# Performance work log

Measured on AMD Instinct MI355X. Metric: run time of the kernel, lower is better.

Reference implementation:

```python
import jax, jax.numpy as jnp
import numpy as np

N = 100_000        # nodes
E = 1_600_000      # edges (avg in-degree 16)
D_IN = 128
D_OUT = 128
K = 2              # hops


def setup_inputs() -> dict:
    key = jax.random.key(0)
    k1, k2, k3, k4 = jax.random.split(key, 4)
    feat = jax.random.normal(k1, (N, D_IN), dtype=jnp.float32)
    src = jax.random.randint(k2, (E,), 0, N, dtype=jnp.int64)
    # guarantee every node has in-degree >= 1 so deg**-0.5 is finite
    # (first N dst entries cover all nodes, rest random)
    dst_rand = jax.random.randint(k3, (E - N,), 0, N, dtype=jnp.int64)
    dst = jnp.concatenate([jnp.arange(N, dtype=jnp.int64), dst_rand])
    # xavier-normal-ish linear params: Linear(D_IN*(K+1) -> D_OUT)
    fan_in = D_IN * (K + 1)
    std = np.sqrt(2.0) * np.sqrt(2.0 / (fan_in + D_OUT))  # gain('relu') * xavier
    W = jax.random.normal(k4, (D_OUT, fan_in), dtype=jnp.float32) * std
    b = jnp.zeros((D_OUT,), dtype=jnp.float32)
    return {"feat": feat, "src": src, "dst": dst, "W": W, "b": b}


def reference(feat, src, dst, W, b):
    n = feat.shape[0]
    # in-degree based symmetric normalization: D^{-1/2} A D^{-1/2}
    deg = jax.ops.segment_sum(jnp.ones_like(dst, dtype=feat.dtype), dst,
                              num_segments=n)
    norm = (deg ** -0.5)[:, None]                 # [N, 1]
    fstack = [feat]
    h = feat
    for _ in range(K):
        h = h * norm                              # pre-scale by D^{-1/2}
        # SpMM: sum of source features into destination nodes
        h = jax.ops.segment_sum(h[src], dst, num_segments=n)
        h = h * norm                              # post-scale by D^{-1/2}
        fstack.append(h)
    x = jnp.concatenate(fstack, axis=-1)          # [N, D_IN*(K+1)]
    return x @ W.T + b
```

## Files before the change

kernel.cpp:

```cpp
#include <hip/hip_runtime.h>
#include <hip/hip_bf16.h>


#define D 128
#define TPB 256
#define GEMM_GRID 768

#define BSH 9
#define BSZ 512
#define NBMAX 256
#define EPT 16
#define CH (TPB * EPT)
#define LCAP 16384

typedef __attribute__((ext_vector_type(8))) short short8;
typedef __attribute__((ext_vector_type(4))) float f32x4;

__device__ __forceinline__ ushort f2bf(float f) {
    unsigned u = __float_as_uint(f);
    u += 0x7fff + ((u >> 16) & 1);
    return (ushort)(u >> 16);
}
__device__ __forceinline__ unsigned pack2bf(float x, float y) {
    return (unsigned)f2bf(x) | ((unsigned)f2bf(y) << 16);
}
__device__ __forceinline__ float bf_lo(unsigned v) { return __uint_as_float(v << 16); }
__device__ __forceinline__ float bf_hi(unsigned v) { return __uint_as_float(v & 0xffff0000u); }

__global__ __launch_bounds__(TPB) void mega_kernel(
    const int* __restrict__ src, const int* __restrict__ dst,
    int* __restrict__ gCursor, unsigned* __restrict__ tmp,
    const float* __restrict__ feat, unsigned* __restrict__ featb,
    const float* __restrict__ W, ushort* __restrict__ Wb,
    int e, int n, int nbin, int npre) {
    __shared__ int hist[NBMAX];
    __shared__ int cellBase[NBMAX];
    int t = threadIdx.x;
    int bid = blockIdx.x;

    if (bid < nbin) {
        hist[t] = 0;
        __syncthreads();
        int base = bid * CH;
        int b[EPT]; unsigned pk[EPT]; int r[EPT];
#pragma unroll
        for (int k = 0; k < EPT; ++k) {
            int i = base + k * TPB + t;
            b[k] = -1;
            if (i < e) {
                int d = dst[i];
                b[k] = d >> BSH;
                pk[k] = ((unsigned)src[i] << BSH) | (unsigned)(d & (BSZ - 1));
                r[k] = atomicAdd(&hist[b[k]], 1);
            }
        }
        __syncthreads();
        int h = hist[t];
        cellBase[t] = h ? t * LCAP + atomicAdd(&gCursor[t], h) : 0;
        __syncthreads();
#pragma unroll
        for (int k = 0; k < EPT; ++k)
            if (b[k] >= 0) tmp[cellBase[b[k]] + r[k]] = pk[k];
    } else if (bid < nbin + npre) {
        int gid = (bid - nbin) * TPB + t;
        int node = gid >> 6, c = gid & 63;
        if (node >= n) return;
        float2 f = ((const float2*)(feat + (size_t)node * D))[c];
        featb[(size_t)node * 64 + c] = pack2bf(f.x, f.y);
    } else {
        int i = ((bid - nbin - npre) * TPB + t) * 4;
        float4 w = *(const float4*)(W + i);
        ushort4 o;
        o.x = f2bf(w.x); o.y = f2bf(w.y); o.z = f2bf(w.z); o.w = f2bf(w.w);
        *(ushort4*)(Wb + i) = o;
    }
}

__global__ __launch_bounds__(TPB) void bucket_csr_kernel(
    const unsigned* __restrict__ tmp, const int* __restrict__ gCursor,
    int2* __restrict__ rsdeg, float* __restrict__ norm, int* __restrict__ csr,
    int n) {
    __shared__ int cnt[BSZ];
    __shared__ int off[BSZ];
    __shared__ int pr[TPB];
    __shared__ int lcsr[LCAP];
    int t = threadIdx.x;
    int bkt = blockIdx.x;
    int beg = bkt * LCAP;
    int m = gCursor[bkt];
    int end = beg + m;
    cnt[t] = 0; cnt[t + TPB] = 0;
    __syncthreads();
    for (int i = beg + t; i < end; i += TPB)
        atomicAdd(&cnt[tmp[i] & (BSZ - 1)], 1);
    __syncthreads();
    int c0 = cnt[2 * t], c1 = cnt[2 * t + 1];
    int own = c0 + c1;
    pr[t] = own;
    __syncthreads();
    for (int o = 1; o < TPB; o <<= 1) {
        int x = (t >= o) ? pr[t - o] : 0;
        __syncthreads();
        pr[t] += x;
        __syncthreads();
    }
    int ex = pr[t] - own;
    off[2 * t] = ex;
    off[2 * t + 1] = ex + c0;
    __syncthreads();
    cnt[t] = 0; cnt[t + TPB] = 0;
    __syncthreads();
    for (int i = beg + t; i < end; i += TPB) {
        unsigned v = tmp[i];
        int l = v & (BSZ - 1);
        int r = atomicAdd(&cnt[l], 1);
        int idx = off[l] + r;
        if (idx < LCAP) lcsr[idx] = (int)(v >> BSH);
    }
    __syncthreads();
    int mm = m < LCAP ? m : LCAP;
    for (int i = t; i < mm; i += TPB) csr[beg + i] = lcsr[i];
    int node0 = bkt << BSH;
    for (int l = t; l < BSZ; l += TPB) {
        int node = node0 + l;
        if (node < n) {
            rsdeg[node] = make_int2(beg + off[l], cnt[l]);
            norm[node] = rsqrtf((float)cnt[l]);
        }
    }
}

__global__ __launch_bounds__(TPB) void spmm_kernel(
    const uint4* __restrict__ hin4, const int2* __restrict__ rsdeg,
    const int* __restrict__ csr, const float* __restrict__ norm,
    unsigned* __restrict__ hout, int n) {
    int w = (blockIdx.x * TPB + threadIdx.x) >> 6;
    if (w >= n) return;
    int lane = threadIdx.x & 63;
    int q = lane >> 4;
    int c = lane & 15;
    int2 rd = rsdeg[w];
    int beg = rd.x, end = rd.x + rd.y;
    float acc[8] = {};
#pragma unroll 4
    for (int j = beg + q; j < end; j += 4) {
        int u = csr[j];
        float s = norm[u];
        uint4 v = hin4[(u << 4) + c];
        acc[0] = fmaf(s, bf_lo(v.x), acc[0]);
        acc[1] = fmaf(s, bf_hi(v.x), acc[1]);
        acc[2] = fmaf(s, bf_lo(v.y), acc[2]);
        acc[3] = fmaf(s, bf_hi(v.y), acc[3]);
        acc[4] = fmaf(s, bf_lo(v.z), acc[4]);
        acc[5] = fmaf(s, bf_hi(v.z), acc[5]);
        acc[6] = fmaf(s, bf_lo(v.w), acc[6]);
        acc[7] = fmaf(s, bf_hi(v.w), acc[7]);
    }
#pragma unroll
    for (int k = 0; k < 8; ++k) {
        acc[k] += __shfl_xor(acc[k], 16, 64);
        acc[k] += __shfl_xor(acc[k], 32, 64);
    }
    if (q == 0) {
        float nv = norm[w];
        uint4 r;
        r.x = pack2bf(acc[0] * nv, acc[1] * nv);
        r.y = pack2bf(acc[2] * nv, acc[3] * nv);
        r.z = pack2bf(acc[4] * nv, acc[5] * nv);
        r.w = pack2bf(acc[6] * nv, acc[7] * nv);
        *(uint4*)(hout + (size_t)w * 64 + c * 4) = r;
    }
}

__global__ __launch_bounds__(TPB) void gemm_mfma_kernel(
    const ushort* __restrict__ featb, const ushort* __restrict__ h1b,
    const ushort* __restrict__ h2b, const ushort* __restrict__ Wb,
    const float* __restrict__ bias, float* __restrict__ out, int n, int ntiles) {
    int lane = threadIdx.x & 63;
    int wave = threadIdx.x >> 6;
    int m = lane & 15, q = lane >> 4;

    short8 b[12][2];
#pragma unroll
    for (int ks = 0; ks < 12; ++ks)
#pragma unroll
        for (int t = 0; t < 2; ++t)
            b[ks][t] = *(const short8*)(Wb + (size_t)(wave * 32 + t * 16 + m) * 384
                                        + ks * 32 + q * 8);
    float bv0 = bias[wave * 32 + m];
    float bv1 = bias[wave * 32 + 16 + m];

    const ushort* srcs[3] = {featb, h1b, h2b};

    for (int tile = blockIdx.x; tile < ntiles; tile += gridDim.x) {
        int row = tile * 16 + m;
        bool va = row < n;
        size_t arow = (size_t)row * D;
        short8 a[12] = {};
        if (va) {
#pragma unroll
            for (int ks = 0; ks < 12; ++ks)
                a[ks] = *(const short8*)(srcs[ks >> 2] + arow + (ks & 3) * 32 + q * 8);
        }
        f32x4 acc0 = {}, acc1 = {};
#pragma unroll
        for (int ks = 0; ks < 12; ++ks) {
            acc0 = __builtin_amdgcn_mfma_f32_16x16x32_bf16(a[ks], b[ks][0], acc0, 0, 0, 0);
            acc1 = __builtin_amdgcn_mfma_f32_16x16x32_bf16(a[ks], b[ks][1], acc1, 0, 0, 0);
        }
        int r0 = tile * 16 + q * 4;
#pragma unroll
        for (int r = 0; r < 4; ++r) {
            int rw = r0 + r;
            if (rw < n) {
                size_t o = (size_t)rw * D + wave * 32 + m;
                out[o] = acc0[r] + bv0;
                out[o + 16] = acc1[r] + bv1;
            }
        }
    }
}

extern "C" void kernel_launch(void* const* d_in, const int* in_sizes, int n_in,
                              void* d_out, int out_size, void* d_ws, size_t ws_size,
                              hipStream_t stream) {
    const float* feat = (const float*)d_in[0];
    const int* src    = (const int*)d_in[1];
    const int* dst    = (const int*)d_in[2];
    const float* W    = (const float*)d_in[3];
    const float* bias = (const float*)d_in[4];
    float* out        = (float*)d_out;

    const int N = in_sizes[0] / D;
    const int E = in_sizes[1];
    const int NB = (N + BSZ - 1) >> BSH;

    char* ws = (char*)d_ws;
    size_t off = 0;
    auto bump = [&](size_t bytes) {
        char* p = ws + off;
        off += (bytes + 255) & ~(size_t)255;
        return p;
    };
    int* gCursor     = (int*)bump((size_t)NBMAX * 4);
    float* norm      = (float*)bump((size_t)N * 4);
    int2* rsdeg      = (int2*)bump((size_t)N * 8);
    unsigned* tmp    = (unsigned*)bump((size_t)NB * LCAP * 4);
    int* csr         = (int*)bump((size_t)NB * LCAP * 4);
    unsigned* featb  = (unsigned*)bump((size_t)N * 64 * 4);
    unsigned* h1b    = (unsigned*)bump((size_t)N * 64 * 4);
    unsigned* h2b    = (unsigned*)bump((size_t)N * 64 * 4);
    ushort* Wb       = (ushort*)bump((size_t)D * 384 * 2);
    (void)ws_size;

    hipMemsetAsync(gCursor, 0, (size_t)NBMAX * 4, stream);

    const int nbin = (E + CH - 1) / CH;
    const int npre = (N * 64 + TPB - 1) / TPB;
    const int nwcv = (D * 384 / 4 + TPB - 1) / TPB;
    mega_kernel<<<nbin + npre + nwcv, TPB, 0, stream>>>(
        src, dst, gCursor, tmp, feat, featb, W, Wb, E, N, nbin, npre);

    bucket_csr_kernel<<<NB, TPB, 0, stream>>>(tmp, gCursor, rsdeg, norm, csr, N);

    const int spmm_blocks = (N * 64 + TPB - 1) / TPB;
    spmm_kernel<<<spmm_blocks, TPB, 0, stream>>>((const uint4*)featb, rsdeg, csr, norm, h1b, N);
    spmm_kernel<<<spmm_blocks, TPB, 0, stream>>>((const uint4*)h1b, rsdeg, csr, norm, h2b, N);

    const int ntiles = (N + 15) / 16;
    gemm_mfma_kernel<<<GEMM_GRID, TPB, 0, stream>>>(
        (const ushort*)featb, (const ushort*)h1b, (const ushort*)h2b,
        Wb, bias, out, N, ntiles);
}
```

Measured before the change: 307.3 us.

## Fuse preprocessing, CSR build and both SpMM hops into one cooperative kernel

Merges the binning, bucket CSR construction and two SpMM passes into a single persistent cooperative kernel separated by grid-wide syncs, replacing the memset and four launches with one launch. The bucket stage now scatters straight to global memory instead of staging 64KB in LDS, which allows higher occupancy (launch bounds 8). Elements per thread in binning are halved. It adds grid.sync costs and grid-stride loops, and falls back to the old multi-kernel path if the cooperative launch fails.

```diff
diff --git a/kernel.cpp b/kernel.cpp
--- a/kernel.cpp
+++ b/kernel.cpp
@@ -1,5 +1,5 @@
 #include <hip/hip_runtime.h>
-#include <hip/hip_bf16.h>
+#include <hip/hip_cooperative_groups.h>
 
 
 #define D 128
@@ -9,9 +9,11 @@
 #define BSH 9
 #define BSZ 512
 #define NBMAX 256
-#define EPT 16
+#define EPT 8
 #define CH (TPB * EPT)
 #define LCAP 16384
+
+namespace cg = cooperative_groups;
 
 typedef __attribute__((ext_vector_type(8))) short short8;
 typedef __attribute__((ext_vector_type(4))) float f32x4;
@@ -27,7 +29,9 @@
 __device__ __forceinline__ float bf_lo(unsigned v) { return __uint_as_float(v << 16); }
 __device__ __forceinline__ float bf_hi(unsigned v) { return __uint_as_float(v & 0xffff0000u); }
 
-__global__ __launch_bounds__(TPB) void mega_kernel(
+
+__device__ __forceinline__ void mega_body(
+    int bid, int t,
     const int* __restrict__ src, const int* __restrict__ dst,
     int* __restrict__ gCursor, unsigned* __restrict__ tmp,
     const float* __restrict__ feat, unsigned* __restrict__ featb,
@@ -35,9 +39,6 @@
     int e, int n, int nbin, int npre) {
     __shared__ int hist[NBMAX];
     __shared__ int cellBase[NBMAX];
-    int t = threadIdx.x;
-    int bid = blockIdx.x;
-
     if (bid < nbin) {
         hist[t] = 0;
         __syncthreads();
@@ -61,12 +62,14 @@
 #pragma unroll
         for (int k = 0; k < EPT; ++k)
             if (b[k] >= 0) tmp[cellBase[b[k]] + r[k]] = pk[k];
+        __syncthreads();
     } else if (bid < nbin + npre) {
         int gid = (bid - nbin) * TPB + t;
         int node = gid >> 6, c = gid & 63;
-        if (node >= n) return;
-        float2 f = ((const float2*)(feat + (size_t)node * D))[c];
-        featb[(size_t)node * 64 + c] = pack2bf(f.x, f.y);
+        if (node < n) {
+            float2 f = ((const float2*)(feat + (size_t)node * D))[c];
+            featb[(size_t)node * 64 + c] = pack2bf(f.x, f.y);
+        }
     } else {
         int i = ((bid - nbin - npre) * TPB + t) * 4;
         float4 w = *(const float4*)(W + i);
@@ -76,16 +79,14 @@
     }
 }
 
-__global__ __launch_bounds__(TPB) void bucket_csr_kernel(
+__device__ __forceinline__ void bucket_body(
+    int bkt, int t,
     const unsigned* __restrict__ tmp, const int* __restrict__ gCursor,
     int2* __restrict__ rsdeg, float* __restrict__ norm, int* __restrict__ csr,
     int n) {
     __shared__ int cnt[BSZ];
     __shared__ int off[BSZ];
     __shared__ int pr[TPB];
-    __shared__ int lcsr[LCAP];
-    int t = threadIdx.x;
-    int bkt = blockIdx.x;
     int beg = bkt * LCAP;
     int m = gCursor[bkt];
     int end = beg + m;
@@ -115,11 +116,9 @@
         int l = v & (BSZ - 1);
         int r = atomicAdd(&cnt[l], 1);
         int idx = off[l] + r;
-        if (idx < LCAP) lcsr[idx] = (int)(v >> BSH);
-    }
-    __syncthreads();
-    int mm = m < LCAP ? m : LCAP;
-    for (int i = t; i < mm; i += TPB) csr[beg + i] = lcsr[i];
+        if (idx < LCAP) csr[beg + idx] = (int)(v >> BSH);
+    }
+    __syncthreads();
     int node0 = bkt << BSH;
     for (int l = t; l < BSZ; l += TPB) {
         int node = node0 + l;
@@ -128,48 +127,105 @@
             norm[node] = rsqrtf((float)cnt[l]);
         }
     }
+    __syncthreads();
+}
+
+__device__ __forceinline__ void spmm_body(
+    const uint4* __restrict__ hin4, const int2* __restrict__ rsdeg,
+    const int* __restrict__ csr, const float* __restrict__ norm,
+    unsigned* __restrict__ hout, int n) {
+    int gw = (int)((blockIdx.x * TPB + threadIdx.x) >> 6);
+    int nw = (int)((gridDim.x * TPB) >> 6);
+    int lane = threadIdx.x & 63;
+    int q = lane >> 4;
+    int c = lane & 15;
+    for (int w = gw; w < n; w += nw) {
+        int2 rd = rsdeg[w];
+        int beg = rd.x, end = rd.x + rd.y;
+        float acc[8] = {};
+#pragma unroll 4
+        for (int j = beg + q; j < end; j += 4) {
+            int u = csr[j];
+            float s = norm[u];
+            uint4 v = hin4[(u << 4) + c];
+            acc[0] = fmaf(s, bf_lo(v.x), acc[0]);
+            acc[1] = fmaf(s, bf_hi(v.x), acc[1]);
+            acc[2] = fmaf(s, bf_lo(v.y), acc[2]);
+            acc[3] = fmaf(s, bf_hi(v.y), acc[3]);
+            acc[4] = fmaf(s, bf_lo(v.z), acc[4]);
+            acc[5] = fmaf(s, bf_hi(v.z), acc[5]);
+            acc[6] = fmaf(s, bf_lo(v.w), acc[6]);
+            acc[7] = fmaf(s, bf_hi(v.w), acc[7]);
+        }
+#pragma unroll
+        for (int k = 0; k < 8; ++k) {
+            acc[k] += __shfl_xor(acc[k], 16, 64);
+            acc[k] += __shfl_xor(acc[k], 32, 64);
+        }
+        if (q == 0) {
+            float nv = norm[w];
+            uint4 r;
+            r.x = pack2bf(acc[0] * nv, acc[1] * nv);
+            r.y = pack2bf(acc[2] * nv, acc[3] * nv);
+            r.z = pack2bf(acc[4] * nv, acc[5] * nv);
+            r.w = pack2bf(acc[6] * nv, acc[7] * nv);
+            *(uint4*)(hout + (size_t)w * 64 + c * 4) = r;
+        }
+    }
+}
+
+__global__ __launch_bounds__(TPB, 8) void fused_kernel(
+    const int* __restrict__ src, const int* __restrict__ dst,
+    int* __restrict__ gCursor, unsigned* __restrict__ tmp,
+    const float* __restrict__ feat, unsigned* __restrict__ featb,
+    const float* __restrict__ W, ushort* __restrict__ Wb,
+    int2* __restrict__ rsdeg, float* __restrict__ norm, int* __restrict__ csr,
+    unsigned* __restrict__ h1b, unsigned* __restrict__ h2b,
+    int e, int n, int nbin, int npre, int nwcv, int nb) {
+    cg::grid_group grid = cg::this_grid();
+    int t = threadIdx.x;
+
+    if (blockIdx.x == 0 && t < NBMAX) gCursor[t] = 0;
+    grid.sync();
+
+    int total1 = nbin + npre + nwcv;
+    for (int bid = blockIdx.x; bid < total1; bid += gridDim.x)
+        mega_body(bid, t, src, dst, gCursor, tmp, feat, featb, W, Wb,
+                  e, n, nbin, npre);
+    grid.sync();
+
+    for (int bkt = blockIdx.x; bkt < nb; bkt += gridDim.x)
+        bucket_body(bkt, t, tmp, gCursor, rsdeg, norm, csr, n);
+    grid.sync();
+
+    spmm_body((const uint4*)featb, rsdeg, csr, norm, h1b, n);
+    grid.sync();
+
+    spmm_body((const uint4*)h1b, rsdeg, csr, norm, h2b, n);
+}
+
+__global__ __launch_bounds__(TPB) void mega_kernel(
+    const int* __restrict__ src, const int* __restrict__ dst,
+    int* __restrict__ gCursor, unsigned* __restrict__ tmp,
+    const float* __restrict__ feat, unsigned* __restrict__ featb,
+    const float* __restrict__ W, ushort* __restrict__ Wb,
+    int e, int n, int nbin, int npre) {
+    mega_body(blockIdx.x, threadIdx.x, src, dst, gCursor, tmp, feat, featb,
+              W, Wb, e, n, nbin, npre);
+}
+
+__global__ __launch_bounds__(TPB) void bucket_csr_kernel(
+    const unsigned* __restrict__ tmp, const int* __restrict__ gCursor,
+    int2* __restrict__ rsdeg, float* __restrict__ norm, int* __restrict__ csr,
+    int n) {
+    bucket_body(blockIdx.x, threadIdx.x, tmp, gCursor, rsdeg, norm, csr, n);
 }
 
 __global__ __launch_bounds__(TPB) void spmm_kernel(
     const uint4* __restrict__ hin4, const int2* __restrict__ rsdeg,
     const int* __restrict__ csr, const float* __restrict__ norm,
     unsigned* __restrict__ hout, int n) {
-    int w = (blockIdx.x * TPB + threadIdx.x) >> 6;
-    if (w >= n) return;
-    int lane = threadIdx.x & 63;
-    int q = lane >> 4;
-    int c = lane & 15;
-    int2 rd = rsdeg[w];
-    int beg = rd.x, end = rd.x + rd.y;
-    float acc[8] = {};
-#pragma unroll 4
-    for (int j = beg + q; j < end; j += 4) {
-        int u = csr[j];
-        float s = norm[u];
-        uint4 v = hin4[(u << 4) + c];
-        acc[0] = fmaf(s, bf_lo(v.x), acc[0]);
-        acc[1] = fmaf(s, bf_hi(v.x), acc[1]);
-        acc[2] = fmaf(s, bf_lo(v.y), acc[2]);
-        acc[3] = fmaf(s, bf_hi(v.y), acc[3]);
-        acc[4] = fmaf(s, bf_lo(v.z), acc[4]);
-        acc[5] = fmaf(s, bf_hi(v.z), acc[5]);
-        acc[6] = fmaf(s, bf_lo(v.w), acc[6]);
-        acc[7] = fmaf(s, bf_hi(v.w), acc[7]);
-    }
-#pragma unroll
-    for (int k = 0; k < 8; ++k) {
-        acc[k] += __shfl_xor(acc[k], 16, 64);
-        acc[k] += __shfl_xor(acc[k], 32, 64);
-    }
-    if (q == 0) {
-        float nv = norm[w];
-        uint4 r;
-        r.x = pack2bf(acc[0] * nv, acc[1] * nv);
-        r.y = pack2bf(acc[2] * nv, acc[3] * nv);
-        r.z = pack2bf(acc[4] * nv, acc[5] * nv);
-        r.w = pack2bf(acc[6] * nv, acc[7] * nv);
-        *(uint4*)(hout + (size_t)w * 64 + c * 4) = r;
-    }
+    spmm_body(hin4, rsdeg, csr, norm, hout, n);
 }
 
 __global__ __launch_bounds__(TPB) void gemm_mfma_kernel(
@@ -231,9 +287,9 @@
     const float* bias = (const float*)d_in[4];
     float* out        = (float*)d_out;
 
-    const int N = in_sizes[0] / D;
-    const int E = in_sizes[1];
-    const int NB = (N + BSZ - 1) >> BSH;
+    int N = in_sizes[0] / D;
+    int E = in_sizes[1];
+    int NB = (N + BSZ - 1) >> BSH;
 
     char* ws = (char*)d_ws;
     size_t off = 0;
@@ -253,19 +309,43 @@
     ushort* Wb       = (ushort*)bump((size_t)D * 384 * 2);
     (void)ws_size;
 
-    hipMemsetAsync(gCursor, 0, (size_t)NBMAX * 4, stream);
-
-    const int nbin = (E + CH - 1) / CH;
-    const int npre = (N * 64 + TPB - 1) / TPB;
-    const int nwcv = (D * 384 / 4 + TPB - 1) / TPB;
-    mega_kernel<<<nbin + npre + nwcv, TPB, 0, stream>>>(
-        src, dst, gCursor, tmp, feat, featb, W, Wb, E, N, nbin, npre);
-
-    bucket_csr_kernel<<<NB, TPB, 0, stream>>>(tmp, gCursor, rsdeg, norm, csr, N);
-
-    const int spmm_blocks = (N * 64 + TPB - 1) / TPB;
-    spmm_kernel<<<spmm_blocks, TPB, 0, stream>>>((const uint4*)featb, rsdeg, csr, norm, h1b, N);
-    spmm_kernel<<<spmm_blocks, TPB, 0, stream>>>((const uint4*)h1b, rsdeg, csr, norm, h2b, N);
+    int nbin = (E + CH - 1) / CH;
+    int npre = (N * 64 + TPB - 1) / TPB;
+    int nwcv = (D * 384 / 4 + TPB - 1) / TPB;
+
+    static int s_mode = 0;
+    static int s_grid = 0;
+    if (s_mode == 0) {
+        int bpc = 0;
+        if (hipOccupancyMaxActiveBlocksPerMultiprocessor(&bpc, fused_kernel,
+                                                         TPB, 0) != hipSuccess ||
+            bpc < 1)
+            bpc = 1;
+        int g = bpc * 256;
+        if (g > 4096) g = 4096;
+        s_grid = g;
+    }
+
+    if (s_mode != 2) {
+        void* args[] = {&src, &dst, &gCursor, &tmp, &feat, &featb, &W, &Wb,
+                        &rsdeg, &norm, &csr, &h1b, &h2b,
+                        &E, &N, &nbin, &npre, &nwcv, &NB};
+        hipError_t le = hipLaunchCooperativeKernel(
+            fused_kernel, dim3(s_grid), dim3(TPB), args, 0u, stream);
+        s_mode = (le == hipSuccess) ? 1 : 2;
+    }
+
+    if (s_mode == 2) {
+        hipMemsetAsync(gCursor, 0, (size_t)NBMAX * 4, stream);
+        mega_kernel<<<nbin + npre + nwcv, TPB, 0, stream>>>(
+            src, dst, gCursor, tmp, feat, featb, W, Wb, E, N, nbin, npre);
+        bucket_csr_kernel<<<NB, TPB, 0, stream>>>(tmp, gCursor, rsdeg, norm, csr, N);
+        const int spmm_blocks = (N * 64 + TPB - 1) / TPB;
+        spmm_kernel<<<spmm_blocks, TPB, 0, stream>>>(
+            (const uint4*)featb, rsdeg, csr, norm, h1b, N);
+        spmm_kernel<<<spmm_blocks, TPB, 0, stream>>>(
+            (const uint4*)h1b, rsdeg, csr, norm, h2b, N);
+    }
 
     const int ntiles = (N + 15) / 16;
     gemm_mfma_kernel<<<GEMM_GRID, TPB, 0, stream>>>(
```

Measured after the change: 774.3 us. 152% more time.
